# Kernel optimization log

Measured on AMD Instinct MI355X. Metric: run time of the kernel, lower is better.

Reference implementation:

```python
import jax, jax.numpy as jnp
import numpy as np

H = 16      # num_attention_heads
D = 128     # head_size
ROT = 32    # rotary_ndims
WIN = 256   # attention_window[layer_id]
G = 64      # max_global_tokens
BASE = 10000.0


def _rotate_half(x):
    x1, x2 = jnp.split(x, 2, axis=-1)
    return jnp.concatenate([-x2, x1], axis=-1)


def setup_inputs() -> dict:
    key = jax.random.key(0)
    ks = jax.random.split(key, 6)
    B, S, HD = 2, 2048, H * D
    hidden_states = jax.random.normal(ks[0], (B, S, HD), jnp.float32)
    attention_mask = jnp.zeros((B, 1, 1, S), jnp.float32)
    glob_idx = jnp.sort(jax.random.randint(ks[1], (B, G), 0, S), axis=-1)
    W_qkv = jax.random.normal(ks[2], (HD, 3 * HD), jnp.float32) * 0.02
    b_qkv = jnp.zeros((3 * HD,), jnp.float32)
    W_o = jax.random.normal(ks[3], (HD, HD), jnp.float32) * 0.02
    b_o = jnp.zeros((HD,), jnp.float32)
    return {"hidden_states": hidden_states, "attention_mask": attention_mask,
            "glob_idx": glob_idx, "W_qkv": W_qkv, "b_qkv": b_qkv,
            "W_o": W_o, "b_o": b_o}


def reference(hidden_states, attention_mask, glob_idx, W_qkv, b_qkv, W_o, b_o):
    B, S, HD = hidden_states.shape
    qkv = (hidden_states @ W_qkv + b_qkv).reshape(B, S, H, 3 * D)
    q = qkv[..., :D].transpose(0, 2, 1, 3)        # [B,H,S,D]
    k = qkv[..., D:2 * D].transpose(0, 2, 1, 3)
    v = qkv[..., 2 * D:].transpose(0, 2, 1, 3)

    # GPT-NeoX rotary on first ROT dims
    inv_freq = 1.0 / (BASE ** (jnp.arange(0, ROT, 2, dtype=jnp.float32) / ROT))
    freqs = jnp.einsum('s,f->sf', jnp.arange(S, dtype=jnp.float32), inv_freq)
    emb = jnp.concatenate([freqs, freqs], axis=-1)           # [S,ROT]
    cos = jnp.cos(emb)[None, None]
    sin = jnp.sin(emb)[None, None]
    q = jnp.concatenate([q[..., :ROT] * cos + _rotate_half(q[..., :ROT]) * sin,
                         q[..., ROT:]], axis=-1)
    k = jnp.concatenate([k[..., :ROT] * cos + _rotate_half(k[..., :ROT]) * sin,
                         k[..., ROT:]], axis=-1)

    # step_attn path: keys/values are head-averaged before attention (key.mean(1))
    k_mean = k.mean(axis=1)   # [B,S,D]
    v_mean = v.mean(axis=1)
    scale = 1.0 / jnp.sqrt(jnp.float32(D))
    minv = jnp.finfo(jnp.float32).min

    s0 = jnp.einsum('bhqd,bkd->bhqk', q[:, :, :WIN], k_mean[:, :WIN]) * scale
    causal = jnp.tril(jnp.ones((WIN, WIN), bool))
    s0 = jnp.where(causal[None, None], s0, minv) + attention_mask[..., :WIN]
    out0 = jnp.einsum('bhqk,bkd->bhqd', jax.nn.softmax(s0, axis=-1), v_mean[:, :WIN])

    Sq = S - WIN
    steps = jnp.arange(Sq)
    win_pos = steps[:, None] + 1 + jnp.arange(WIN)[None, :]
    k_win = k_mean[:, win_pos]
    v_win = v_mean[:, win_pos]
    mask_win = attention_mask[:, 0, 0, :][:, win_pos][:, None]
    qs = q[:, :, WIN:]                                        # [B,H,Sq,D]
    s_win = jnp.einsum('bhqd,bqwd->bhqw', qs, k_win) * scale + mask_win

    k_glob = jnp.take_along_axis(k_mean, glob_idx[..., None], axis=1)  # [B,G,D]
    v_glob = jnp.take_along_axis(v_mean, glob_idx[..., None], axis=1)
    # sorted indices: 'filter < i then truncate to G' == prefix-valid mask per slot
    valid = (glob_idx[:, None, :] < steps[None, :, None])[:, None]     # [B,1,Sq,G]
    s_glob = jnp.where(valid, jnp.einsum('bhqd,bgd->bhqg', qs, k_glob) * scale, minv)

    w = jax.nn.softmax(jnp.concatenate([s_glob, s_win], axis=-1), axis=-1)
    out_steps = (jnp.einsum('bhqg,bgd->bhqd', w[..., :G], v_glob)
                 + jnp.einsum('bhqw,bqwd->bhqd', w[..., G:], v_win))

    out = jnp.concatenate([out0, out_steps], axis=2)          # [B,H,S,D]
    out = out.transpose(0, 2, 1, 3).reshape(B, S, HD)
    return out @ W_o + b_o
```

## Files before the change

### kernel.cpp

```cpp
#include <hip/hip_runtime.h>
#include <math.h>

#define SCALE_ 0.08838834764831845f
#define MINV_  (-3.4028234663852886e38f)

typedef __bf16 bf16;
typedef bf16  bf16x4 __attribute__((ext_vector_type(4)));
typedef bf16  bf16x8 __attribute__((ext_vector_type(8)));
typedef float f32x4  __attribute__((ext_vector_type(4)));
typedef float f32x16 __attribute__((ext_vector_type(16)));
typedef float float4v __attribute__((ext_vector_type(4)));

#define LD8(p) (*(const bf16x8*)(p))

__device__ __forceinline__ f32x4 mfma16(bf16x8 a, bf16x8 b, f32x4 c) {
    return __builtin_amdgcn_mfma_f32_16x16x32_bf16(a, b, c, 0, 0, 0);
}
__device__ __forceinline__ f32x16 mfma32(bf16x8 a, bf16x8 b, f32x16 c) {
    return __builtin_amdgcn_mfma_f32_32x32x16_bf16(a, b, c, 0, 0, 0);
}

typedef const __attribute__((address_space(1))) void* gas_t;
typedef __attribute__((address_space(3))) void* sas_t;
__device__ __forceinline__ void gload_lds16(const void* g, void* l) {
    __builtin_amdgcn_global_load_lds((gas_t)g, (sas_t)l, 16, 0, 0);
}


__global__ __launch_bounds__(256) void cast_hidden_kernel(const float* __restrict__ X, bf16* __restrict__ Y)
{
    int i = (blockIdx.x * 256 + threadIdx.x) * 4;
    float4v v = *(const float4v*)(X + i);
    bf16x4 o; o.x = (bf16)v.x; o.y = (bf16)v.y; o.z = (bf16)v.z; o.w = (bf16)v.w;
    *(bf16x4*)(Y + i) = o;
}

__global__ __launch_bounds__(256) void transpose_cast_kernel(const float* __restrict__ W, bf16* __restrict__ BT,
                                                             int srcStride, int qmap)
{
    __shared__ float tile[32][33];
    int k0 = blockIdx.x * 32, n0 = blockIdx.y * 32;
    int c = threadIdx.x & 31, r = threadIdx.x >> 5;
    int n = n0 + c;
    int src = qmap ? ((n >> 7) * 384 + (n & 127)) : n;
    #pragma unroll
    for (int rr = 0; rr < 32; rr += 8)
        tile[r + rr][c] = W[(size_t)(k0 + r + rr) * srcStride + src];
    __syncthreads();
    #pragma unroll
    for (int rr = 0; rr < 32; rr += 8)
        BT[(size_t)(n0 + r + rr) * 2048 + k0 + c] = (bf16)tile[c][r + rr];
}

__global__ __launch_bounds__(256) void bt1_kv_kernel(const float* __restrict__ Wqkv, bf16* __restrict__ BT1)
{
    int k0 = blockIdx.x * 16;
    int j = threadIdx.x;
    float acc[16];
    #pragma unroll
    for (int k = 0; k < 16; k++) acc[k] = 0.f;
    for (int h = 0; h < 16; h++) {
        #pragma unroll
        for (int k = 0; k < 16; k++)
            acc[k] += Wqkv[(size_t)(k0 + k) * 6144 + h * 384 + 128 + j];
    }
    #pragma unroll
    for (int k = 0; k < 16; k++)
        BT1[(size_t)(2048 + j) * 2048 + k0 + k] = (bf16)(acc[k] * 0.0625f);
}

__global__ void bias1_kernel(const float* __restrict__ bqkv, float* __restrict__ bias1)
{
    int c = blockIdx.x * 256 + threadIdx.x;
    if (c >= 2304) return;
    if (c < 2048) bias1[c] = bqkv[(c >> 7) * 384 + (c & 127)];
    else {
        int j = c - 2048; float s = 0.f;
        for (int h = 0; h < 16; h++) s += bqkv[h * 384 + 128 + j];
        bias1[c] = s * 0.0625f;
    }
}

template<int OUT_BF16>
__global__ __launch_bounds__(256) void gemm_kernel(const bf16* __restrict__ A, const bf16* __restrict__ BT,
                                                   const float* __restrict__ bias, void* __restrict__ Cout,
                                                   int M, int N, int K)
{
    __shared__ __align__(16) bf16 As[128 * 64];
    __shared__ __align__(16) bf16 Bs[128 * 64];
    const int tid  = threadIdx.x;
    const int wv   = tid >> 6, lane = tid & 63, l32 = lane & 31, half = lane >> 5;
    const int wrow = wv >> 1, wcol = wv & 1;
    const int m0 = blockIdx.y * 128, n0 = blockIdx.x * 128;

    int rowS[4], colS[4];
    #pragma unroll
    for (int j = 0; j < 4; j++) {
        int flat = (wv * 4 + j) * 64 + lane;
        int row = flat >> 3, cp = flat & 7;
        rowS[j] = row;
        colS[j] = (cp ^ (row & 7)) * 8;
    }

    f32x16 acc[2][2];
    #pragma unroll
    for (int i = 0; i < 2; i++)
        #pragma unroll
        for (int j = 0; j < 2; j++)
            #pragma unroll
            for (int r = 0; r < 16; r++) acc[i][j][r] = 0.f;

    for (int kk = 0; kk < K; kk += 64) {
        __syncthreads();
        #pragma unroll
        for (int j = 0; j < 4; j++) {
            gload_lds16(A  + (size_t)(m0 + rowS[j]) * K + kk + colS[j], &As[(wv * 4 + j) * 512]);
            gload_lds16(BT + (size_t)(n0 + rowS[j]) * K + kk + colS[j], &Bs[(wv * 4 + j) * 512]);
        }
        __syncthreads();

        bf16x8 af[2][4], bfr[2][4];
        #pragma unroll
        for (int mt = 0; mt < 2; mt++) {
            int row = wrow * 64 + mt * 32 + l32;
            #pragma unroll
            for (int k16 = 0; k16 < 4; k16++) {
                int lc = k16 * 2 + half;
                af[mt][k16] = LD8(&As[row * 64 + ((lc ^ (row & 7)) * 8)]);
            }
        }
        #pragma unroll
        for (int nt = 0; nt < 2; nt++) {
            int row = wcol * 64 + nt * 32 + l32;
            #pragma unroll
            for (int k16 = 0; k16 < 4; k16++) {
                int lc = k16 * 2 + half;
                bfr[nt][k16] = LD8(&Bs[row * 64 + ((lc ^ (row & 7)) * 8)]);
            }
        }
        #pragma unroll
        for (int k16 = 0; k16 < 4; k16++)
            #pragma unroll
            for (int mt = 0; mt < 2; mt++)
                #pragma unroll
                for (int nt = 0; nt < 2; nt++)
                    acc[mt][nt] = mfma32(af[mt][k16], bfr[nt][k16], acc[mt][nt]);
    }

    #pragma unroll
    for (int mt = 0; mt < 2; mt++) {
        #pragma unroll
        for (int nt = 0; nt < 2; nt++) {
            int n = n0 + wcol * 64 + nt * 32 + l32;
            float bn = bias[n];
            #pragma unroll
            for (int r = 0; r < 16; r++) {
                int m = m0 + wrow * 64 + mt * 32 + (r & 3) + 8 * (r >> 2) + 4 * half;
                float v = acc[mt][nt][r] + bn;
                if (OUT_BF16) ((bf16*)Cout)[(size_t)m * N + n] = (bf16)v;
                else          ((float*)Cout)[(size_t)m * N + n] = v;
            }
        }
    }
}

__global__ __launch_bounds__(320) void rotary_kernel(bf16* __restrict__ C1)
{
    int row = blockIdx.x;
    int s = row & 2047;
    int t = threadIdx.x;
    if (t >= 272) return;
    int g = t >> 4, dd = t & 15;
    bf16* ptr = C1 + (size_t)row * 2304 + (g < 16 ? g * 128 : 2048);
    float x0 = (float)ptr[dd], x1 = (float)ptr[dd + 16];
    const float L = 0.575646273248511f;
    float inv = __expf(-L * (float)dd);
    float ang = (float)s * inv;
    float c, si;
    __sincosf(ang, &si, &c);
    ptr[dd]      = (bf16)(x0 * c - x1 * si);
    ptr[dd + 16] = (bf16)(x1 * c + x0 * si);
}

__global__ __launch_bounds__(256) void build_vmT_kernel(const bf16* __restrict__ C1, bf16* __restrict__ vmT)
{
    __shared__ float tile[32][33];
    int b = blockIdx.z;
    int s0 = blockIdx.x * 32, d0 = blockIdx.y * 32;
    int c = threadIdx.x & 31, r = threadIdx.x >> 5;
    #pragma unroll
    for (int rr = 0; rr < 32; rr += 8)
        tile[r + rr][c] = (float)C1[(size_t)(b * 2048 + s0 + r + rr) * 2304 + 2176 + d0 + c];
    __syncthreads();
    #pragma unroll
    for (int rr = 0; rr < 32; rr += 8)
        vmT[(size_t)(b * 128 + d0 + r + rr) * 2048 + s0 + c] = (bf16)tile[c][r + rr];
}

__global__ __launch_bounds__(256) void pretile_kernel(const bf16* __restrict__ C1, const bf16* __restrict__ vmT,
                                                      const int* __restrict__ gidx,
                                                      bf16* __restrict__ KF, bf16* __restrict__ VF)
{
    int c = blockIdx.x, b = blockIdx.y;
    bool isGlob = (c == 32);
    for (int i = 0; i < 8; i++) {
        int sid = threadIdx.x + i * 256;
        int lane = sid & 63, fi = (sid >> 6) & 15;
        int l16 = lane & 15, quad = lane >> 4;
        if (sid < 1024) {
            int t = fi >> 2, ks = fi & 3;
            int pos = isGlob ? gidx[b * 64 + t * 16 + l16] : (c * 64 + t * 16 + l16);
            const bf16* src = C1 + (size_t)(b * 2048 + pos) * 2304 + 2048 + ks * 32 + quad * 8;
            *(bf16x8*)&KF[((size_t)(b * 33 + c) * 16 + fi) * 512 + lane * 8] = LD8(src);
        } else {
            int dt = fi >> 1, ks2 = fi & 1;
            int d = dt * 16 + l16;
            if (isGlob) {
                bf16 tmp[8];
                #pragma unroll
                for (int j = 0; j < 8; j++) {
                    int pos = gidx[b * 64 + ks2 * 32 + quad * 8 + j];
                    tmp[j] = vmT[(size_t)(b * 128 + d) * 2048 + pos];
                }
                #pragma unroll
                for (int j = 0; j < 8; j++)
                    VF[((size_t)(b * 33 + 32) * 16 + fi) * 512 + lane * 8 + j] = tmp[j];
            } else {
                const bf16* src = vmT + (size_t)(b * 128 + d) * 2048 + c * 64 + ks2 * 32 + quad * 8;
                *(bf16x8*)&VF[((size_t)(b * 33 + c) * 16 + fi) * 512 + lane * 8] = LD8(src);
            }
        }
    }
}

#define PSTRIDE 88

__global__ __launch_bounds__(256) void attn0_kernel(const bf16* __restrict__ C1, const bf16* __restrict__ KF,
                                                    const bf16* __restrict__ VF, const float* __restrict__ mask,
                                                    bf16* __restrict__ attn)
{
    const int bx = blockIdx.x, h = blockIdx.y, b = blockIdx.z;
    const int tid = threadIdx.x, wv = tid >> 6, lane = tid & 63, quad = lane >> 4, l16 = lane & 15;
    const int q0 = (bx * 4 + wv) * 16;

    __shared__ __align__(16) bf16 Ps[4 * 16 * PSTRIDE];
    bf16* Pw = &Ps[wv * (16 * PSTRIDE)];

    bf16x8 af[4];
    const bf16* qbase = C1 + (size_t)(b * 2048 + q0 + l16) * 2304 + h * 128;
    #pragma unroll
    for (int ks = 0; ks < 4; ks++) af[ks] = LD8(qbase + ks * 32 + quad * 8);

    f32x4 m_run = (f32x4){MINV_, MINV_, MINV_, MINV_};
    f32x4 l_run = (f32x4){0.f, 0.f, 0.f, 0.f};
    f32x4 O[8];
    #pragma unroll
    for (int dt = 0; dt < 8; dt++) O[dt] = (f32x4){0.f, 0.f, 0.f, 0.f};

    for (int c = 0; c <= bx; c++) {
        const bf16* KFc = KF + ((size_t)(b * 33 + c) * 16) * 512;
        const bf16* VFc = VF + ((size_t)(b * 33 + c) * 16) * 512;

        f32x4 acc[4];
        #pragma unroll
        for (int t = 0; t < 4; t++) acc[t] = (f32x4){0.f, 0.f, 0.f, 0.f};
        #pragma unroll
        for (int t = 0; t < 4; t++)
            #pragma unroll
            for (int ks = 0; ks < 4; ks++)
                acc[t] = mfma16(af[ks], LD8(KFc + (size_t)(t * 4 + ks) * 512 + lane * 8), acc[t]);

        float sv[4][4];
        #pragma unroll
        for (int t = 0; t < 4; t++) {
            int key = c * 64 + t * 16 + l16;
            float addv = mask[b * 2048 + key];
            #pragma unroll
            for (int r = 0; r < 4; r++) {
                int q = q0 + quad * 4 + r;
                sv[t][r] = (key <= q) ? (acc[t][r] * SCALE_ + addv) : MINV_;
            }
        }

        f32x4 cm;
        #pragma unroll
        for (int r = 0; r < 4; r++) cm[r] = fmaxf(fmaxf(sv[0][r], sv[1][r]), fmaxf(sv[2][r], sv[3][r]));
        #pragma unroll
        for (int ms = 1; ms < 16; ms <<= 1)
            #pragma unroll
            for (int r = 0; r < 4; r++) cm[r] = fmaxf(cm[r], __shfl_xor(cm[r], ms, 64));

        f32x4 nm, alpha;
        #pragma unroll
        for (int r = 0; r < 4; r++) { nm[r] = fmaxf(m_run[r], cm[r]); alpha[r] = __expf(m_run[r] - nm[r]); }

        float pv[4][4];
        f32x4 cs = (f32x4){0.f, 0.f, 0.f, 0.f};
        #pragma unroll
        for (int t = 0; t < 4; t++)
            #pragma unroll
            for (int r = 0; r < 4; r++) {
                pv[t][r] = __expf(sv[t][r] - nm[r]);
                cs[r] += pv[t][r];
            }
        #pragma unroll
        for (int ms = 1; ms < 16; ms <<= 1)
            #pragma unroll
            for (int r = 0; r < 4; r++) cs[r] += __shfl_xor(cs[r], ms, 64);

        m_run = nm;
        #pragma unroll
        for (int r = 0; r < 4; r++) l_run[r] = l_run[r] * alpha[r] + cs[r];
        #pragma unroll
        for (int dt = 0; dt < 8; dt++)
            #pragma unroll
            for (int r = 0; r < 4; r++) O[dt][r] *= alpha[r];

        #pragma unroll
        for (int t = 0; t < 4; t++)
            #pragma unroll
            for (int r = 0; r < 4; r++)
                Pw[(quad * 4 + r) * PSTRIDE + t * 16 + l16] = (bf16)pv[t][r];
        bf16x8 pa0 = LD8(&Pw[l16 * PSTRIDE + quad * 8]);
        bf16x8 pa1 = LD8(&Pw[l16 * PSTRIDE + 32 + quad * 8]);

        #pragma unroll
        for (int dt = 0; dt < 8; dt++) {
            O[dt] = mfma16(pa0, LD8(VFc + (size_t)(dt * 2 + 0) * 512 + lane * 8), O[dt]);
            O[dt] = mfma16(pa1, LD8(VFc + (size_t)(dt * 2 + 1) * 512 + lane * 8), O[dt]);
        }
    }

    f32x4 invl;
    #pragma unroll
    for (int r = 0; r < 4; r++) invl[r] = 1.0f / l_run[r];
    #pragma unroll
    for (int dt = 0; dt < 8; dt++)
        #pragma unroll
        for (int r = 0; r < 4; r++) {
            int q = q0 + quad * 4 + r;
            attn[(size_t)(b * 2048 + q) * 2048 + h * 128 + dt * 16 + l16] = (bf16)(O[dt][r] * invl[r]);
        }
}

__global__ __launch_bounds__(256) void attn_steps3_kernel(const bf16* __restrict__ C1, const bf16* __restrict__ KF,
                                                          const bf16* __restrict__ VF, const float* __restrict__ mask,
                                                          const int* __restrict__ gidx, bf16* __restrict__ attn)
{
    const int sb = blockIdx.x, b = blockIdx.y;
    const int tid = threadIdx.x, wv = tid >> 6, lane = tid & 63, quad = lane >> 4, l16 = lane & 15;
    const int step = sb * 4 + wv, p = 256 + step;

    __shared__ __align__(16) bf16 Ps[4 * 16 * PSTRIDE];
    bf16* Pw = &Ps[wv * (16 * PSTRIDE)];

    bf16x8 af[4];
    const bf16* qrow = C1 + (size_t)(b * 2048 + p) * 2304;
    #pragma unroll
    for (int ks = 0; ks < 4; ks++) af[ks] = LD8(qrow + l16 * 128 + ks * 32 + quad * 8);

    int gix[4];
    #pragma unroll
    for (int t = 0; t < 4; t++) gix[t] = gidx[b * 64 + t * 16 + l16];

    f32x4 m_run = (f32x4){MINV_, MINV_, MINV_, MINV_};
    f32x4 l_run = (f32x4){0.f, 0.f, 0.f, 0.f};
    f32x4 O[8];
    #pragma unroll
    for (int dt = 0; dt < 8; dt++) O[dt] = (f32x4){0.f, 0.f, 0.f, 0.f};

    const int c0 = (step + 1) >> 6;

    for (int iter = 0; iter < 6; iter++) {
        int c;
        bool isGlob = (iter == 0);
        if (isGlob) c = 32;
        else { c = c0 + iter - 1; if (c > 31) break; }

        const bf16* KFc = KF + ((size_t)(b * 33 + c) * 16) * 512;
        const bf16* VFc = VF + ((size_t)(b * 33 + c) * 16) * 512;

        f32x4 acc[4];
        #pragma unroll
        for (int t = 0; t < 4; t++) acc[t] = (f32x4){0.f, 0.f, 0.f, 0.f};
        #pragma unroll
        for (int t = 0; t < 4; t++)
            #pragma unroll
            for (int ks = 0; ks < 4; ks++)
                acc[t] = mfma16(af[ks], LD8(KFc + (size_t)(t * 4 + ks) * 512 + lane * 8), acc[t]);

        float sv[4][4];
        bool vld[4];
        #pragma unroll
        for (int t = 0; t < 4; t++) {
            float addv = 0.f;
            if (isGlob) vld[t] = gix[t] < step;
            else {
                int pos = c * 64 + t * 16 + l16;
                vld[t] = (unsigned)(pos - step - 1) < 256u;
                addv = mask[b * 2048 + pos];
            }
            #pragma unroll
            for (int r = 0; r < 4; r++) sv[t][r] = vld[t] ? (acc[t][r] * SCALE_ + addv) : MINV_;
        }

        f32x4 cm;
        #pragma unroll
        for (int r = 0; r < 4; r++) cm[r] = fmaxf(fmaxf(sv[0][r], sv[1][r]), fmaxf(sv[2][r], sv[3][r]));
        #pragma unroll
        for (int ms = 1; ms < 16; ms <<= 1)
            #pragma unroll
            for (int r = 0; r < 4; r++) cm[r] = fmaxf(cm[r], __shfl_xor(cm[r], ms, 64));

        f32x4 nm, alpha;
        #pragma unroll
        for (int r = 0; r < 4; r++) { nm[r] = fmaxf(m_run[r], cm[r]); alpha[r] = __expf(m_run[r] - nm[r]); }

        float pv[4][4];
        f32x4 cs = (f32x4){0.f, 0.f, 0.f, 0.f};
        #pragma unroll
        for (int t = 0; t < 4; t++)
            #pragma unroll
            for (int r = 0; r < 4; r++) {
                pv[t][r] = vld[t] ? __expf(sv[t][r] - nm[r]) : 0.f;
                cs[r] += pv[t][r];
            }
        #pragma unroll
        for (int ms = 1; ms < 16; ms <<= 1)
            #pragma unroll
            for (int r = 0; r < 4; r++) cs[r] += __shfl_xor(cs[r], ms, 64);

        m_run = nm;
        #pragma unroll
        for (int r = 0; r < 4; r++) l_run[r] = l_run[r] * alpha[r] + cs[r];
        #pragma unroll
        for (int dt = 0; dt < 8; dt++)
            #pragma unroll
            for (int r = 0; r < 4; r++) O[dt][r] *= alpha[r];

        #pragma unroll
        for (int t = 0; t < 4; t++)
            #pragma unroll
            for (int r = 0; r < 4; r++)
                Pw[(quad * 4 + r) * PSTRIDE + t * 16 + l16] = (bf16)pv[t][r];
        bf16x8 pa0 = LD8(&Pw[l16 * PSTRIDE + quad * 8]);
        bf16x8 pa1 = LD8(&Pw[l16 * PSTRIDE + 32 + quad * 8]);

        #pragma unroll
        for (int dt = 0; dt < 8; dt++) {
            O[dt] = mfma16(pa0, LD8(VFc + (size_t)(dt * 2 + 0) * 512 + lane * 8), O[dt]);
            O[dt] = mfma16(pa1, LD8(VFc + (size_t)(dt * 2 + 1) * 512 + lane * 8), O[dt]);
        }
    }

    f32x4 invl;
    #pragma unroll
    for (int r = 0; r < 4; r++) invl[r] = 1.0f / l_run[r];
    #pragma unroll
    for (int dt = 0; dt < 8; dt++)
        #pragma unroll
        for (int r = 0; r < 4; r++) {
            int h = quad * 4 + r;
            attn[(size_t)(b * 2048 + p) * 2048 + h * 128 + dt * 16 + l16] = (bf16)(O[dt][r] * invl[r]);
        }
}

extern "C" void kernel_launch(void* const* d_in, const int* in_sizes, int n_in,
                              void* d_out, int out_size, void* d_ws, size_t ws_size,
                              hipStream_t stream)
{
    const float* hidden = (const float*)d_in[0];
    const float* amask  = (const float*)d_in[1];
    const int*   gidx   = (const int*)d_in[2];
    const float* Wqkv   = (const float*)d_in[3];
    const float* bqkv   = (const float*)d_in[4];
    const float* Wo     = (const float*)d_in[5];
    const float* bo     = (const float*)d_in[6];

    char* ws = (char*)d_ws;
    size_t off = 0;
    auto take = [&](size_t bytes) -> char* {
        char* p = ws + off;
        off = (off + bytes + 255) & ~(size_t)255;
        return p;
    };
    bf16*  A16   = (bf16*)take(4096ull * 2048 * 2);
    bf16*  BT1   = (bf16*)take(2304ull * 2048 * 2);
    bf16*  BT2   = (bf16*)take(2048ull * 2048 * 2);
    bf16*  C1    = (bf16*)take(4096ull * 2304 * 2);
    bf16*  vmT   = (bf16*)take(2ull * 128 * 2048 * 2);
    bf16*  KF    = (bf16*)take(2ull * 33 * 16 * 512 * 2);
    bf16*  VF    = (bf16*)take(2ull * 33 * 16 * 512 * 2);
    bf16*  attnb = (bf16*)take(4096ull * 2048 * 2);
    float* bias1 = (float*)take(2304 * 4);

    cast_hidden_kernel<<<8192, 256, 0, stream>>>(hidden, A16);
    transpose_cast_kernel<<<dim3(64, 64), 256, 0, stream>>>(Wqkv, BT1, 6144, 1);
    bt1_kv_kernel<<<128, 256, 0, stream>>>(Wqkv, BT1);
    bias1_kernel<<<9, 256, 0, stream>>>(bqkv, bias1);
    transpose_cast_kernel<<<dim3(64, 64), 256, 0, stream>>>(Wo, BT2, 2048, 0);

    gemm_kernel<1><<<dim3(18, 32), 256, 0, stream>>>(A16, BT1, bias1, (void*)C1, 4096, 2304, 2048);

    rotary_kernel<<<4096, 320, 0, stream>>>(C1);
    build_vmT_kernel<<<dim3(64, 4, 2), 256, 0, stream>>>(C1, vmT);
    pretile_kernel<<<dim3(33, 2), 256, 0, stream>>>(C1, vmT, gidx, KF, VF);

    attn0_kernel<<<dim3(4, 16, 2), 256, 0, stream>>>(C1, KF, VF, amask, attnb);
    attn_steps3_kernel<<<dim3(448, 2), 256, 0, stream>>>(C1, KF, VF, amask, gidx, attnb);

    gemm_kernel<0><<<dim3(16, 32), 256, 0, stream>>>(attnb, BT2, bo, d_out, 4096, 2048, 2048);

    (void)in_sizes; (void)n_in; (void)out_size; (void)ws_size;
}
```

Measured before the change: 321.0 us.

## Shrink GEMM tiles to 128x64 with grouped block swizzle and higher occupancy

The GEMM tile changes from 128x128 to 128x64, with each wave owning a 32-row strip across both N subtiles. Blocks are launched on a 1D grid and remapped in groups of four M-tiles so neighbouring blocks share A rows for better L2 reuse. Launch bounds now request 4 blocks per CU, and the LDS footprint is smaller. The aim is to fix the low block count on 256 CUs (576 and 512 blocks before), at the cost of less register-level reuse per MFMA and extra B-tile global traffic.

```diff
diff --git a/kernel.cpp b/kernel.cpp
--- a/kernel.cpp
+++ b/kernel.cpp
@@ -82,56 +82,59 @@
 }
 
 template<int OUT_BF16>
-__global__ __launch_bounds__(256) void gemm_kernel(const bf16* __restrict__ A, const bf16* __restrict__ BT,
-                                                   const float* __restrict__ bias, void* __restrict__ Cout,
-                                                   int M, int N, int K)
+__global__ __launch_bounds__(256, 4) void gemm_kernel(const bf16* __restrict__ A, const bf16* __restrict__ BT,
+                                                      const float* __restrict__ bias, void* __restrict__ Cout,
+                                                      int N, int K, int nTiles, int nbTot)
 {
     __shared__ __align__(16) bf16 As[128 * 64];
-    __shared__ __align__(16) bf16 Bs[128 * 64];
+    __shared__ __align__(16) bf16 Bs[64 * 64];
     const int tid  = threadIdx.x;
     const int wv   = tid >> 6, lane = tid & 63, l32 = lane & 31, half = lane >> 5;
-    const int wrow = wv >> 1, wcol = wv & 1;
-    const int m0 = blockIdx.y * 128, n0 = blockIdx.x * 128;
-
-    int rowS[4], colS[4];
-    #pragma unroll
-    for (int j = 0; j < 4; j++) {
-        int flat = (wv * 4 + j) * 64 + lane;
-        int row = flat >> 3, cp = flat & 7;
+
+    int b = blockIdx.x;
+    int group = b / (4 * nTiles), rem = b % (4 * nTiles);
+    int mi = group * 4 + (rem & 3), ni = rem >> 2;
+    const int m0 = mi * 128, n0 = ni * 64;
+
+    int ciS[6], rowS[6], colS[6];
+    #pragma unroll
+    for (int j = 0; j < 6; j++) {
+        int ci = wv * 6 + j;
+        ciS[j] = ci;
+        int cb = (ci < 16) ? ci : (ci - 16);
+        int row = cb * 8 + (lane >> 3), cp = lane & 7;
         rowS[j] = row;
         colS[j] = (cp ^ (row & 7)) * 8;
     }
 
-    f32x16 acc[2][2];
-    #pragma unroll
-    for (int i = 0; i < 2; i++)
-        #pragma unroll
-        for (int j = 0; j < 2; j++)
-            #pragma unroll
-            for (int r = 0; r < 16; r++) acc[i][j][r] = 0.f;
+    f32x16 acc[2];
+    #pragma unroll
+    for (int t = 0; t < 2; t++)
+        #pragma unroll
+        for (int r = 0; r < 16; r++) acc[t][r] = 0.f;
 
     for (int kk = 0; kk < K; kk += 64) {
         __syncthreads();
         #pragma unroll
-        for (int j = 0; j < 4; j++) {
-            gload_lds16(A  + (size_t)(m0 + rowS[j]) * K + kk + colS[j], &As[(wv * 4 + j) * 512]);
-            gload_lds16(BT + (size_t)(n0 + rowS[j]) * K + kk + colS[j], &Bs[(wv * 4 + j) * 512]);
+        for (int j = 0; j < 6; j++) {
+            int ci = ciS[j];
+            if (ci < 16) gload_lds16(A  + (size_t)(m0 + rowS[j]) * K + kk + colS[j], &As[ci * 512]);
+            else         gload_lds16(BT + (size_t)(n0 + rowS[j]) * K + kk + colS[j], &Bs[(ci - 16) * 512]);
         }
         __syncthreads();
 
-        bf16x8 af[2][4], bfr[2][4];
-        #pragma unroll
-        for (int mt = 0; mt < 2; mt++) {
-            int row = wrow * 64 + mt * 32 + l32;
+        bf16x8 af[4], bfr[2][4];
+        {
+            int row = wv * 32 + l32;
             #pragma unroll
             for (int k16 = 0; k16 < 4; k16++) {
                 int lc = k16 * 2 + half;
-                af[mt][k16] = LD8(&As[row * 64 + ((lc ^ (row & 7)) * 8)]);
+                af[k16] = LD8(&As[row * 64 + ((lc ^ (row & 7)) * 8)]);
             }
         }
         #pragma unroll
         for (int nt = 0; nt < 2; nt++) {
-            int row = wcol * 64 + nt * 32 + l32;
+            int row = nt * 32 + l32;
             #pragma unroll
             for (int k16 = 0; k16 < 4; k16++) {
                 int lc = k16 * 2 + half;
@@ -141,25 +144,20 @@
         #pragma unroll
         for (int k16 = 0; k16 < 4; k16++)
             #pragma unroll
-            for (int mt = 0; mt < 2; mt++)
-                #pragma unroll
-                for (int nt = 0; nt < 2; nt++)
-                    acc[mt][nt] = mfma32(af[mt][k16], bfr[nt][k16], acc[mt][nt]);
-    }
-
-    #pragma unroll
-    for (int mt = 0; mt < 2; mt++) {
-        #pragma unroll
-        for (int nt = 0; nt < 2; nt++) {
-            int n = n0 + wcol * 64 + nt * 32 + l32;
-            float bn = bias[n];
-            #pragma unroll
-            for (int r = 0; r < 16; r++) {
-                int m = m0 + wrow * 64 + mt * 32 + (r & 3) + 8 * (r >> 2) + 4 * half;
-                float v = acc[mt][nt][r] + bn;
-                if (OUT_BF16) ((bf16*)Cout)[(size_t)m * N + n] = (bf16)v;
-                else          ((float*)Cout)[(size_t)m * N + n] = v;
-            }
+            for (int nt = 0; nt < 2; nt++)
+                acc[nt] = mfma32(af[k16], bfr[nt][k16], acc[nt]);
+    }
+
+    #pragma unroll
+    for (int nt = 0; nt < 2; nt++) {
+        int n = n0 + nt * 32 + l32;
+        float bn = bias[n];
+        #pragma unroll
+        for (int r = 0; r < 16; r++) {
+            int m = m0 + wv * 32 + (r & 3) + 8 * (r >> 2) + 4 * half;
+            float v = acc[nt][r] + bn;
+            if (OUT_BF16) ((bf16*)Cout)[(size_t)m * N + n] = (bf16)v;
+            else          ((float*)Cout)[(size_t)m * N + n] = v;
         }
     }
 }
@@ -500,7 +498,7 @@
     bias1_kernel<<<9, 256, 0, stream>>>(bqkv, bias1);
     transpose_cast_kernel<<<dim3(64, 64), 256, 0, stream>>>(Wo, BT2, 2048, 0);
 
-    gemm_kernel<1><<<dim3(18, 32), 256, 0, stream>>>(A16, BT1, bias1, (void*)C1, 4096, 2304, 2048);
+    gemm_kernel<1><<<1152, 256, 0, stream>>>(A16, BT1, bias1, (void*)C1, 2304, 2048, 36, 1152);
 
     rotary_kernel<<<4096, 320, 0, stream>>>(C1);
     build_vmT_kernel<<<dim3(64, 4, 2), 256, 0, stream>>>(C1, vmT);
@@ -509,7 +507,7 @@
     attn0_kernel<<<dim3(4, 16, 2), 256, 0, stream>>>(C1, KF, VF, amask, attnb);
     attn_steps3_kernel<<<dim3(448, 2), 256, 0, stream>>>(C1, KF, VF, amask, gidx, attnb);
 
-    gemm_kernel<0><<<dim3(16, 32), 256, 0, stream>>>(attnb, BT2, bo, d_out, 4096, 2048, 2048);
+    gemm_kernel<0><<<1024, 256, 0, stream>>>(attnb, BT2, bo, d_out, 2048, 2048, 32, 1024);
 
     (void)in_sizes; (void)n_in; (void)out_size; (void)ws_size;
 }
```

New measurement: 333.2 us. 3.8% more time.
